# Kernel optimization log

Measured on AMD Instinct MI355X. Metric: run time of the kernel, lower is better.

## Reference

```python
import jax, jax.numpy as jnp
import numpy as np

N = 100000   # nodes
E = 400000   # edges
B = 4000     # graphs
D = 300      # emb_dim
L = 5        # num_layer
MAX_LEN = 50 # max_atom_num (hard-coded in forward)
SELF_LOOP_BOND_TYPE = 4
BN_EPS = 1e-5


def setup_inputs() -> dict:
    key = jax.random.key(0)
    ks = jax.random.split(key, 12)
    x = jax.random.randint(ks[0], (N, 2), 0, 3)            # col0 atom type (<120), col1 chirality (<3)
    edge_index = jax.random.randint(ks[1], (2, E), 0, N)
    edge_attr = jax.random.randint(ks[2], (E, 2), 0, 3)    # col0 bond type (<6), col1 direction (<3)
    batch = jnp.sort(jax.random.randint(ks[3], (N,), 0, B))
    sc = 0.05
    x_emb1 = jax.random.normal(ks[4], (120, D)) * sc
    x_emb2 = jax.random.normal(ks[5], (3, D)) * sc
    e_emb1 = jax.random.normal(ks[6], (L, 6, D)) * sc
    e_emb2 = jax.random.normal(ks[7], (L, 3, D)) * sc
    W1 = jax.random.normal(ks[8], (L, D, 2 * D)) * (1.0 / np.sqrt(D))
    b1 = jnp.zeros((L, 2 * D))
    W2 = jax.random.normal(ks[9], (L, 2 * D, D)) * (1.0 / np.sqrt(2 * D))
    b2 = jnp.zeros((L, D))
    bn_gamma = jnp.ones((L, D))
    bn_beta = jnp.zeros((L, D))
    return dict(x=x, edge_index=edge_index, edge_attr=edge_attr, batch=batch,
                num_graphs=B, x_emb1=x_emb1, x_emb2=x_emb2, e_emb1=e_emb1,
                e_emb2=e_emb2, W1=W1, b1=b1, W2=W2, b2=b2,
                bn_gamma=bn_gamma, bn_beta=bn_beta)


def reference(x, edge_index, edge_attr, batch, num_graphs,
              x_emb1, x_emb2, e_emb1, e_emb2, W1, b1, W2, b2, bn_gamma, bn_beta):
    n = x.shape[0]
    # input node embedding: atom type + chirality
    h = x_emb1[x[:, 0]] + x_emb2[x[:, 1]]  # [N, D]
    # add self loops (bond_type=4, direction=0)
    loop = jnp.arange(n)
    src = jnp.concatenate([edge_index[0], loop])
    dst = jnp.concatenate([edge_index[1], loop])
    ea0 = jnp.concatenate([edge_attr[:, 0], jnp.full((n,), SELF_LOOP_BOND_TYPE, edge_attr.dtype)])
    ea1 = jnp.concatenate([edge_attr[:, 1], jnp.zeros((n,), edge_attr.dtype)])
    num_layers = W1.shape[0]
    for l in range(num_layers):
        ee = e_emb1[l][ea0] + e_emb2[l][ea1]                 # [E+N, D] edge embeddings
        msg = h[src] + ee                                     # gather + message
        agg = jax.ops.segment_sum(msg, dst, num_segments=n)   # scatter-add aggregation
        hid = jax.nn.relu(agg @ W1[l] + b1[l])                # GIN MLP
        h2 = hid @ W2[l] + b2[l]
        mean = h2.mean(axis=0)                                # BatchNorm1d (batch stats, biased var)
        var = jnp.mean((h2 - mean) ** 2, axis=0)
        h2 = (h2 - mean) * jax.lax.rsqrt(var + BN_EPS) * bn_gamma[l] + bn_beta[l]
        # dropout with drop_ratio=0 is identity; relu on all but last layer
        h = h2 if l == num_layers - 1 else jax.nn.relu(h2)
    # global mean pool over graphs
    counts = jax.ops.segment_sum(jnp.ones((n,), h.dtype), batch, num_segments=num_graphs)
    pooled = jax.ops.segment_sum(h, batch, num_segments=num_graphs) / jnp.maximum(counts, 1.0)[:, None]
    # atom_feature_pad: pad per-graph node features to MAX_LEN with mask
    idx = jnp.arange(n)
    is_start = jnp.concatenate([jnp.array([True]), batch[1:] != batch[:-1]])
    start = jax.lax.cummax(jnp.where(is_start, idx, 0))
    pos = idx - start                                          # position within each graph
    valid = pos < MAX_LEN
    posc = jnp.minimum(pos, MAX_LEN - 1)
    d = h.shape[1]
    node_feature = jnp.zeros((num_graphs, MAX_LEN, d), h.dtype).at[batch, posc].add(
        h * valid[:, None].astype(h.dtype))
    mask = jnp.zeros((num_graphs, MAX_LEN), h.dtype).at[batch, posc].add(valid.astype(h.dtype))
    return pooled, node_feature, mask
```

## Files before the change

kernel.cpp:

```cpp
#include <hip/hip_runtime.h>
#include <cstdint>

#define D 300
#define MAXLEN 50
#define K1P 320
#define H1 600
#define H1P 608
#define W1ROWS 640
#define W2ROWS 384

typedef __attribute__((ext_vector_type(8))) short s16x8;
typedef __attribute__((ext_vector_type(4))) short s16x4;
typedef __attribute__((ext_vector_type(4))) float f32x4;
typedef __attribute__((ext_vector_type(2))) float f32x2;
typedef __attribute__((ext_vector_type(4))) int i32x4;

__device__ __forceinline__ unsigned short f2b(float f) {
  uint32_t u = __builtin_bit_cast(uint32_t, f);
  u += 0x7FFFu + ((u >> 16) & 1u);
  return (unsigned short)(u >> 16);
}
__device__ __forceinline__ float b2f(unsigned short s) {
  return __builtin_bit_cast(float, (uint32_t)s << 16);
}
__device__ __forceinline__ void gld_lds16(const void* g, void* l) {
  __builtin_amdgcn_global_load_lds((const __attribute__((address_space(1))) void*)g,
                                   (__attribute__((address_space(3))) void*)l, 16, 0, 0);
}

__global__ void k_cmb(const float* __restrict__ xe1, const float* __restrict__ xe2,
                      unsigned short* __restrict__ cmb, int total ) {
  int i = blockIdx.x * blockDim.x + threadIdx.x;
  if (i >= total) return;
  int c = i / 75, d = (i - c * 75) * 4;
  int a = c / 3, b = c - a * 3;
  s16x4 out;
#pragma unroll
  for (int j = 0; j < 4; ++j) out[j] = (short)f2b(xe1[(size_t)a * D + d + j] + xe2[(size_t)b * D + d + j]);
  *(s16x4*)(cmb + (size_t)c * K1P + d) = out;
}

__global__ void k_cid(const int* __restrict__ x, int* __restrict__ cid, int N) {
  int i = blockIdx.x * blockDim.x + threadIdx.x;
  if (i < N) cid[i] = x[2 * i] * 3 + x[2 * i + 1];
}

__global__ void k_count(const int* __restrict__ key, int* __restrict__ cnt, int n) {
  int i = blockIdx.x * blockDim.x + threadIdx.x;
  if (i < n) atomicAdd(&cnt[key[i]], 1);
}

__global__ void k_scan1(const int* __restrict__ in, int* __restrict__ part, int n) {
  __shared__ int red[256];
  int tid = threadIdx.x;
  int base = blockIdx.x * 1024 + tid * 4;
  i32x4 v = {0, 0, 0, 0};
  if (base + 3 < n) v = *(const i32x4*)(in + base);
  else {
#pragma unroll
    for (int k = 0; k < 4; ++k) v[k] = (base + k < n) ? in[base + k] : 0;
  }
  int s = v[0] + v[1] + v[2] + v[3];
  red[tid] = s;
  __syncthreads();
  for (int off = 1; off < 256; off <<= 1) {
    int t = (tid >= off) ? red[tid - off] : 0;
    __syncthreads();
    red[tid] += t;
    __syncthreads();
  }
  if (tid == 255) part[blockIdx.x] = red[255];
}

__global__ void k_scan2(int* __restrict__ part, int P) {
  __shared__ int sm[1024];
  int tid = threadIdx.x;
  int v = (tid < P) ? part[tid] : 0;
  sm[tid] = v;
  __syncthreads();
  for (int off = 1; off < 1024; off <<= 1) {
    int t = (tid >= off) ? sm[tid - off] : 0;
    __syncthreads();
    sm[tid] += t;
    __syncthreads();
  }
  if (tid < P) part[tid] = sm[tid] - v;
  if (tid == 1023) part[P] = sm[1023];
}

__global__ void k_scan3(const int* __restrict__ in, const int* __restrict__ part,
                        int* __restrict__ out, int n, int P) {
  __shared__ int red[256];
  int tid = threadIdx.x;
  int base = blockIdx.x * 1024 + tid * 4;
  i32x4 v = {0, 0, 0, 0};
  if (base + 3 < n) v = *(const i32x4*)(in + base);
  else {
#pragma unroll
    for (int k = 0; k < 4; ++k) v[k] = (base + k < n) ? in[base + k] : 0;
  }
  int s = v[0] + v[1] + v[2] + v[3];
  red[tid] = s;
  __syncthreads();
  for (int off = 1; off < 256; off <<= 1) {
    int t = (tid >= off) ? red[tid - off] : 0;
    __syncthreads();
    red[tid] += t;
    __syncthreads();
  }
  int pre = red[tid] - s + part[blockIdx.x];
  if (base < n) out[base] = pre;
  if (base + 1 < n) out[base + 1] = pre + v[0];
  if (base + 2 < n) out[base + 2] = pre + v[0] + v[1];
  if (base + 3 < n) out[base + 3] = pre + v[0] + v[1] + v[2];
  if (blockIdx.x == 0 && tid == 0) out[n] = part[P];
}

__global__ void k_fill(const int* __restrict__ src, const int* __restrict__ dst,
                       const int* __restrict__ ea, const int* __restrict__ cid,
                       int* __restrict__ cur, const int* __restrict__ offs,
                       int* __restrict__ ssrc, int* __restrict__ scid,
                       int* __restrict__ cnt18, int E_) {
  int e = blockIdx.x * blockDim.x + threadIdx.x;
  if (e >= E_) return;
  int d = dst[e];
  int s = src[e];
  int p = atomicAdd(&cur[d], 1);
  int pos = offs[d] + p;
  ssrc[pos] = s;
  scid[pos] = cid[s];
  int co = ea[2 * e] * 3 + ea[2 * e + 1];
  atomicAdd(&cnt18[d * 18 + co], 1);
}

__global__ void k_cnt18bf(const int* __restrict__ cnt18, unsigned short* __restrict__ aggbf, int N) {
  int idx = blockIdx.x * blockDim.x + threadIdx.x;
  if (idx >= N * 10) return;
  int i = idx / 10, j = idx - i * 10;
  uint32_t o = 0;
  if (j < 9) {
    int c0 = cnt18[i * 18 + 2 * j] + (2 * j == 12 ? 1 : 0);
    int c1 = cnt18[i * 18 + 2 * j + 1];
    o = (uint32_t)f2b((float)c0) | ((uint32_t)f2b((float)c1) << 16);
  }
  *(uint32_t*)(aggbf + (size_t)i * K1P + D + j * 2) = o;
}

__global__ void k_ecw1(const float* __restrict__ ee1, const float* __restrict__ ee2,
                       const float* __restrict__ W1, unsigned short* __restrict__ W1tA,
                       int L_, int total ) {
  int idx = blockIdx.x * blockDim.x + threadIdx.x;
  if (idx >= total) return;
  int k18 = idx % 18;
  int n = (idx / 18) % H1;
  int l = idx / (18 * H1);
  const float* e1 = ee1 + ((size_t)l * 6 + k18 / 3) * D;
  const float* e2 = ee2 + ((size_t)l * 3 + k18 % 3) * D;
  const float* w = W1 + (size_t)l * D * H1 + n;
  float s = 0.f;
  for (int d = 0; d < D; ++d) s += (e1[d] + e2[d]) * w[(size_t)d * H1];
  W1tA[(size_t)l * W1ROWS * K1P + (size_t)n * K1P + D + k18] = f2b(s);
}

template <int FUSE>
__global__ void k_agg(const unsigned short* __restrict__ hin, const int* __restrict__ ridx,
                      const int* __restrict__ offs, const float* __restrict__ scale,
                      const float* __restrict__ shift, const int* __restrict__ selfcid,
                      unsigned short* __restrict__ aggbf, int N) {
  int w = (int)((blockIdx.x * blockDim.x + threadIdx.x) >> 6);
  if (w >= N) return;
  int lane = threadIdx.x & 63;
  const bool act1 = lane < 11;
  const int e0 = lane * 4;
  const int e1 = (act1 ? (64 + lane) : lane) * 4;
  float sc0[4], sh0[4], sc1[4], sh1[4];
  if (FUSE) {
    f32x4 a = *(const f32x4*)(scale + e0);
    f32x4 b = *(const f32x4*)(shift + e0);
    f32x4 c = *(const f32x4*)(scale + e1);
    f32x4 d = *(const f32x4*)(shift + e1);
#pragma unroll
    for (int j = 0; j < 4; ++j) { sc0[j] = a[j]; sh0[j] = b[j]; sc1[j] = c[j]; sh1[j] = d[j]; }
  } else {
#pragma unroll
    for (int j = 0; j < 4; ++j) { sc0[j] = sc1[j] = sh0[j] = sh1[j] = 0.f; }
  }
  int beg = offs[w], end = offs[w + 1];
  int wrow = FUSE ? w : selfcid[w];
  float s0[4], s1[4];
  {
    const unsigned short* rp = hin + (size_t)wrow * K1P;
    s16x4 v0 = *(const s16x4*)(rp + e0);
    s16x4 v1 = *(const s16x4*)(rp + e1);
#pragma unroll
    for (int j = 0; j < 4; ++j) {
      float a = b2f((unsigned short)v0[j]);
      float b = b2f((unsigned short)v1[j]);
      if (FUSE) { a = fmaxf(a * sc0[j] + sh0[j], 0.f); b = fmaxf(b * sc1[j] + sh1[j], 0.f); }
      s0[j] = a; s1[j] = b;
    }
  }
  int j = beg;
  for (; j + 4 <= end; j += 4) {
    const unsigned short* p0 = hin + (size_t)ridx[j] * K1P;
    const unsigned short* p1 = hin + (size_t)ridx[j + 1] * K1P;
    const unsigned short* p2 = hin + (size_t)ridx[j + 2] * K1P;
    const unsigned short* p3 = hin + (size_t)ridx[j + 3] * K1P;
    s16x4 a0 = *(const s16x4*)(p0 + e0), b0 = *(const s16x4*)(p0 + e1);
    s16x4 a1 = *(const s16x4*)(p1 + e0), b1 = *(const s16x4*)(p1 + e1);
    s16x4 a2 = *(const s16x4*)(p2 + e0), b2 = *(const s16x4*)(p2 + e1);
    s16x4 a3 = *(const s16x4*)(p3 + e0), b3 = *(const s16x4*)(p3 + e1);
#pragma unroll
    for (int k = 0; k < 4; ++k) {
      float x0 = b2f((unsigned short)a0[k]), x1 = b2f((unsigned short)a1[k]);
      float x2 = b2f((unsigned short)a2[k]), x3 = b2f((unsigned short)a3[k]);
      float y0 = b2f((unsigned short)b0[k]), y1 = b2f((unsigned short)b1[k]);
      float y2 = b2f((unsigned short)b2[k]), y3 = b2f((unsigned short)b3[k]);
      if (FUSE) {
        x0 = fmaxf(x0 * sc0[k] + sh0[k], 0.f); x1 = fmaxf(x1 * sc0[k] + sh0[k], 0.f);
        x2 = fmaxf(x2 * sc0[k] + sh0[k], 0.f); x3 = fmaxf(x3 * sc0[k] + sh0[k], 0.f);
        y0 = fmaxf(y0 * sc1[k] + sh1[k], 0.f); y1 = fmaxf(y1 * sc1[k] + sh1[k], 0.f);
        y2 = fmaxf(y2 * sc1[k] + sh1[k], 0.f); y3 = fmaxf(y3 * sc1[k] + sh1[k], 0.f);
      }
      s0[k] += (x0 + x1) + (x2 + x3);
      s1[k] += (y0 + y1) + (y2 + y3);
    }
  }
  for (; j < end; ++j) {
    const unsigned short* rp = hin + (size_t)ridx[j] * K1P;
    s16x4 v0 = *(const s16x4*)(rp + e0);
    s16x4 v1 = *(const s16x4*)(rp + e1);
#pragma unroll
    for (int k = 0; k < 4; ++k) {
      float a = b2f((unsigned short)v0[k]);
      float b = b2f((unsigned short)v1[k]);
      if (FUSE) { a = fmaxf(a * sc0[k] + sh0[k], 0.f); b = fmaxf(b * sc1[k] + sh1[k], 0.f); }
      s0[k] += a;
      s1[k] += b;
    }
  }
  s16x4 o0, o1;
#pragma unroll
  for (int k = 0; k < 4; ++k) { o0[k] = (short)f2b(s0[k]); o1[k] = (short)f2b(s1[k]); }
  *(s16x4*)(aggbf + (size_t)w * K1P + e0) = o0;
  if (act1) *(s16x4*)(aggbf + (size_t)w * K1P + e1) = o1;
}

__global__ void k_wconv(const float* __restrict__ W, unsigned short* __restrict__ Wt,
                        int K, int Nout, int Kp, int total) {
  int idx = blockIdx.x * blockDim.x + threadIdx.x;
  if (idx >= total) return;
  int n = idx / Kp, k = idx - n * Kp;
  float v = (k < K && n < Nout) ? W[(size_t)k * Nout + n] : 0.f;
  Wt[idx] = f2b(v);
}

template <int K, int EPI>
__global__ __launch_bounds__(256, 3) void k_gemm(
    const unsigned short* __restrict__ A, const unsigned short* __restrict__ Bt,
    const float* __restrict__ bias, unsigned short* __restrict__ Cb,
    float* __restrict__ sums, int M, int Nout, int ldc, int CT) {
  constexpr int T = K / 32;
  __shared__ __align__(16) unsigned short smem[24576];

  int nwg = gridDim.x;
  int q = nwg >> 3, r8 = nwg & 7;
  int xcd = blockIdx.x & 7, oidx = blockIdx.x >> 3;
  int wid = (xcd < r8 ? xcd * (q + 1) : r8 * (q + 1) + (xcd - r8) * q) + oidx;
  int ct = wid % CT, rt = wid / CT;
  const int rowBase = rt * 128, colBase = ct * 128;

  const int tid = threadIdx.x, lane = tid & 63, wave = tid >> 6;
  const int wm = wave >> 1, wn = wave & 1;
  const int l15 = lane & 15, lg = lane >> 4;

  unsigned short* Asm = smem;
  unsigned short* Bsm = smem + 12288;

  auto stage = [&](int s, int t) {
#pragma unroll
    for (int i = 0; i < 2; ++i) {
      int u = tid + i * 256;
      int rr = u >> 2;
      int cdat = (u & 3) ^ ((rr >> 1) & 3);
      int gr = rowBase + rr; if (gr >= M) gr = M - 1;
      gld_lds16(A + (size_t)gr * K + t * 32 + cdat * 8, Asm + s * 4096 + u * 8);
      gld_lds16(Bt + (size_t)(colBase + rr) * K + t * 32 + cdat * 8, Bsm + s * 4096 + u * 8);
    }
  };

  f32x4 acc[4][4] = {};
  stage(0, 0);
  stage(1, 1);
#pragma unroll
  for (int t = 0; t < T; ++t) {
    if (t + 1 < T) asm volatile("s_waitcnt vmcnt(4)" ::: "memory");
    else           asm volatile("s_waitcnt vmcnt(0)" ::: "memory");
    __builtin_amdgcn_s_barrier();
    __builtin_amdgcn_sched_barrier(0);
    const unsigned short* bA = Asm + (t % 3) * 4096;
    const unsigned short* bB = Bsm + (t % 3) * 4096;
    s16x8 af[4], bf[4];
#pragma unroll
    for (int i = 0; i < 4; ++i) {
      int ra = wm * 64 + i * 16 + l15;
      int rb = wn * 64 + i * 16 + l15;
      af[i] = *(const s16x8*)(bA + ((size_t)ra * 4 + (lg ^ ((ra >> 1) & 3))) * 8);
      bf[i] = *(const s16x8*)(bB + ((size_t)rb * 4 + (lg ^ ((rb >> 1) & 3))) * 8);
    }
    if (t + 2 < T) stage((t + 2) % 3, t + 2);
#pragma unroll
    for (int mi = 0; mi < 4; ++mi)
#pragma unroll
      for (int ni = 0; ni < 4; ++ni)
        acc[mi][ni] = __builtin_amdgcn_mfma_f32_16x16x32_bf16(af[mi], bf[ni], acc[mi][ni], 0, 0, 0);
  }

  float bnS[4] = {0.f, 0.f, 0.f, 0.f}, bnQ[4] = {0.f, 0.f, 0.f, 0.f};
#pragma unroll
  for (int ni = 0; ni < 4; ++ni) {
    int col = colBase + wn * 64 + ni * 16 + l15;
    if (col >= (EPI ? ldc : Nout)) continue;
    bool inN = col < Nout;
    float bv = inN ? bias[col] : 0.f;
#pragma unroll
    for (int mi = 0; mi < 4; ++mi) {
      int row0 = rowBase + wm * 64 + mi * 16 + lg * 4;
#pragma unroll
      for (int rr = 0; rr < 4; ++rr) {
        int row = row0 + rr;
        if (row < M) {
          float v = inN ? acc[mi][ni][rr] + bv : 0.f;
          if (EPI) v = fmaxf(v, 0.f);
          else { bnS[ni] += v; bnQ[ni] += v * v; }
          Cb[(size_t)row * ldc + col] = f2b(v);
        }
      }
    }
  }
  if (!EPI) {
#pragma unroll
    for (int ni = 0; ni < 4; ++ni) {
      float cs = bnS[ni], cq = bnQ[ni];
      cs += __shfl_xor(cs, 16); cq += __shfl_xor(cq, 16);
      cs += __shfl_xor(cs, 32); cq += __shfl_xor(cq, 32);
      int col = colBase + wn * 64 + ni * 16 + l15;
      if (lg == 0 && col < Nout) {
        atomicAdd(&sums[col], cs);
        atomicAdd(&sums[D + col], cq);
      }
    }
  }
}

__global__ void k_bnfinal(const float* __restrict__ sums, const float* __restrict__ sumsq,
                          const float* __restrict__ gamma, const float* __restrict__ beta,
                          float* __restrict__ scale, float* __restrict__ shift, int N) {
  int c = threadIdx.x;
  if (c >= D) return;
  float inv = 1.f / (float)N;
  float mean = sums[c] * inv;
  float var = sumsq[c] * inv - mean * mean;
  if (var < 0.f) var = 0.f;
  float sc = gamma[c] * rsqrtf(var + 1e-5f);
  scale[c] = sc;
  shift[c] = beta[c] - mean * sc;
}

__global__ void k_pool(const unsigned short* __restrict__ hb, const float* __restrict__ scale,
                       const float* __restrict__ shift, const int* __restrict__ gs,
                       const int* __restrict__ gc, float* __restrict__ pooled, int total ) {
  int gid = blockIdx.x * blockDim.x + threadIdx.x;
  if (gid >= total) return;
  int g = gid / 75, c4 = (gid - g * 75) * 4;
  int start = gs[g], cnt = gc[g];
  f32x4 s = {0.f, 0.f, 0.f, 0.f};
  for (int i = 0; i < cnt; ++i) {
    s16x4 in = *(const s16x4*)(hb + (size_t)(start + i) * K1P + c4);
#pragma unroll
    for (int j = 0; j < 4; ++j) s[j] += b2f((unsigned short)in[j]);
  }
  f32x4 sc = *(const f32x4*)(scale + c4);
  f32x4 sh = *(const f32x4*)(shift + c4);
  float dv = (cnt > 0) ? (float)cnt : 1.f;
  f32x4 out;
#pragma unroll
  for (int j = 0; j < 4; ++j) out[j] = (s[j] * sc[j] + sh[j] * (float)cnt) / dv;
  *(f32x4*)(pooled + (size_t)g * D + c4) = out;
}

__global__ void k_nf(const unsigned short* __restrict__ hb, const float* __restrict__ scale,
                     const float* __restrict__ shift, const int* __restrict__ gs,
                     const int* __restrict__ gc, float* __restrict__ nf, float* __restrict__ mask) {
  int g = blockIdx.x;
  int start = gs[g], cnt = gc[g];
  int lim = cnt < MAXLEN ? cnt : MAXLEN;
  for (int idx = threadIdx.x; idx < MAXLEN * 75; idx += 256) {
    int p = idx / 75;
    int c4 = (idx - p * 75) * 4;
    f32x4 v = {0.f, 0.f, 0.f, 0.f};
    if (p < lim) {
      s16x4 in = *(const s16x4*)(hb + (size_t)(start + p) * K1P + c4);
      f32x4 sc = *(const f32x4*)(scale + c4);
      f32x4 sh = *(const f32x4*)(shift + c4);
#pragma unroll
      for (int j = 0; j < 4; ++j) v[j] = b2f((unsigned short)in[j]) * sc[j] + sh[j];
    }
    *(f32x4*)(nf + (size_t)g * (MAXLEN * D) + p * D + c4) = v;
  }
  if (threadIdx.x < MAXLEN) mask[(size_t)g * MAXLEN + threadIdx.x] = (threadIdx.x < lim) ? 1.f : 0.f;
}

extern "C" void kernel_launch(void* const* d_in, const int* in_sizes, int n_in,
                              void* d_out, int out_size, void* d_ws, size_t ws_size,
                              hipStream_t stream) {
  const int* x      = (const int*)d_in[0];
  const int* ei     = (const int*)d_in[1];
  const int* ea     = (const int*)d_in[2];
  const int* batch  = (const int*)d_in[3];
  const float* xe1  = (const float*)d_in[5];
  const float* xe2  = (const float*)d_in[6];
  const float* ee1  = (const float*)d_in[7];
  const float* ee2  = (const float*)d_in[8];
  const float* W1   = (const float*)d_in[9];
  const float* b1   = (const float*)d_in[10];
  const float* W2   = (const float*)d_in[11];
  const float* b2   = (const float*)d_in[12];
  const float* gamma = (const float*)d_in[13];
  const float* beta  = (const float*)d_in[14];

  const int N = in_sizes[0] / 2;
  const int E = in_sizes[1] / 2;
  const int L = in_sizes[9] / (D * 2 * D);
  const int B = out_size / (D + MAXLEN * D + MAXLEN);

  char* ws = (char*)d_ws;
  size_t off = 0;
  auto alloc = [&](size_t bytes) -> void* {
    void* p = ws + off;
    off += (bytes + 255) & ~(size_t)255;
    return p;
  };
  unsigned short* aggbf = (unsigned short*)alloc((size_t)N * K1P * 2);
  unsigned short* hb    = (unsigned short*)alloc((size_t)N * K1P * 2);
  unsigned short* hid   = (unsigned short*)alloc((size_t)N * H1P * 2);
  unsigned short* cmb   = (unsigned short*)alloc((size_t)360 * K1P * 2);
  unsigned short* W1tA = (unsigned short*)alloc((size_t)L * W1ROWS * K1P * 2);
  unsigned short* W2tA = (unsigned short*)alloc((size_t)L * W2ROWS * H1P * 2);
  int* cnt    = (int*)alloc((size_t)N * 4);
  int* cur    = (int*)alloc((size_t)N * 4);
  int* offs   = (int*)alloc((size_t)(N + 1) * 4);
  int* cid    = (int*)alloc((size_t)N * 4);
  int* cnt18  = (int*)alloc((size_t)N * 18 * 4);
  int* ssrc   = (int*)alloc((size_t)E * 4);
  int* scid   = (int*)alloc((size_t)E * 4);
  int* gc     = (int*)alloc((size_t)B * 4);
  int* gs     = (int*)alloc((size_t)(B + 1) * 4);
  int* part   = (int*)alloc(1024 * 4);
  float* sumsA = (float*)alloc((size_t)L * 2 * D * 4);
  float* scale = (float*)alloc(2 * D * 4);

  hipMemsetAsync(cnt, 0, (size_t)N * 4, stream);
  hipMemsetAsync(cur, 0, (size_t)N * 4, stream);
  hipMemsetAsync(gc, 0, (size_t)B * 4, stream);
  hipMemsetAsync(cnt18, 0, (size_t)N * 18 * 4, stream);
  hipMemsetAsync(sumsA, 0, (size_t)L * 2 * D * 4, stream);

  k_cmb<<<(360 * 75 + 255) / 256, 256, 0, stream>>>(xe1, xe2, cmb, 360 * 75);
  k_cid<<<(N + 255) / 256, 256, 0, stream>>>(x, cid, N);
  k_count<<<(E + 255) / 256, 256, 0, stream>>>(ei + E, cnt, E);
  {
    int P = (N + 1023) / 1024;
    k_scan1<<<P, 256, 0, stream>>>(cnt, part, N);
    k_scan2<<<1, 1024, 0, stream>>>(part, P);
    k_scan3<<<P, 256, 0, stream>>>(cnt, part, offs, N, P);
  }
  k_fill<<<(E + 255) / 256, 256, 0, stream>>>(ei, ei + E, ea, cid, cur, offs, ssrc, scid, cnt18, E);
  k_cnt18bf<<<(N * 10 + 255) / 256, 256, 0, stream>>>(cnt18, aggbf, N);
  k_count<<<(N + 255) / 256, 256, 0, stream>>>(batch, gc, N);
  {
    int P = (B + 1023) / 1024;
    k_scan1<<<P, 256, 0, stream>>>(gc, part, B);
    k_scan2<<<1, 1024, 0, stream>>>(part, P);
    k_scan3<<<P, 256, 0, stream>>>(gc, part, gs, B, P);
  }
  for (int l = 0; l < L; ++l) {
    k_wconv<<<(W1ROWS * K1P + 255) / 256, 256, 0, stream>>>(
        W1 + (size_t)l * D * H1, W1tA + (size_t)l * W1ROWS * K1P, D, H1, K1P, W1ROWS * K1P);
    k_wconv<<<(W2ROWS * H1P + 255) / 256, 256, 0, stream>>>(
        W2 + (size_t)l * H1 * D, W2tA + (size_t)l * W2ROWS * H1P, H1, D, H1P, W2ROWS * H1P);
  }
  k_ecw1<<<(L * H1 * 18 + 255) / 256, 256, 0, stream>>>(ee1, ee2, W1, W1tA, L, L * H1 * 18);

  const int RT = (N + 127) / 128;
  for (int l = 0; l < L; ++l) {
    float* sums = sumsA + (size_t)l * 2 * D;
    if (l == 0)
      k_agg<0><<<(N + 3) / 4, 256, 0, stream>>>(cmb, scid, offs, nullptr, nullptr, cid, aggbf, N);
    else
      k_agg<1><<<(N + 3) / 4, 256, 0, stream>>>(hb, ssrc, offs, scale, scale + D, nullptr, aggbf, N);
    k_gemm<K1P, 1><<<5 * RT, 256, 0, stream>>>(
        aggbf, W1tA + (size_t)l * W1ROWS * K1P, b1 + (size_t)l * H1, hid, nullptr, N, H1, H1P, 5);
    k_gemm<H1P, 0><<<3 * RT, 256, 0, stream>>>(
        hid, W2tA + (size_t)l * W2ROWS * H1P, b2 + (size_t)l * D, hb, sums, N, D, K1P, 3);
    k_bnfinal<<<1, 320, 0, stream>>>(sums, sums + D, gamma + (size_t)l * D, beta + (size_t)l * D,
                                     scale, scale + D, N);
  }

  float* out = (float*)d_out;
  float* out_pooled = out;
  float* out_nf = out + (size_t)B * D;
  float* out_mask = out + (size_t)B * D + (size_t)B * MAXLEN * D;
  k_pool<<<(B * 75 + 255) / 256, 256, 0, stream>>>(hb, scale, scale + D, gs, gc, out_pooled, B * 75);
  k_nf<<<B, 256, 0, stream>>>(hb, scale, scale + D, gs, gc, out_nf, out_mask);
}
```

Baseline: 1.676 ms.

## Load GEMM A operand directly from global into registers, bypassing LDS

The A tile in the MFMA GEMM was staged through LDS with global-to-LDS copies. It is now loaded per lane straight from global memory into registers, double-buffered two k-steps ahead, while B keeps the triple-buffered LDS path. This halves LDS traffic and footprint, which may allow more resident blocks. In exchange, A rows are re-fetched by both wn waves, global reads become less coalesced (16 bytes per lane per row), and the vmcnt wait accounting changes.

```diff
diff --git a/kernel.cpp b/kernel.cpp
--- a/kernel.cpp
+++ b/kernel.cpp
@@ -261,7 +261,7 @@
     const float* __restrict__ bias, unsigned short* __restrict__ Cb,
     float* __restrict__ sums, int M, int Nout, int ldc, int CT) {
   constexpr int T = K / 32;
-  __shared__ __align__(16) unsigned short smem[24576];
+  __shared__ __align__(16) unsigned short Bsm[3 * 4096];
 
   int nwg = gridDim.x;
   int q = nwg >> 3, r8 = nwg & 7;
@@ -274,46 +274,56 @@
   const int wm = wave >> 1, wn = wave & 1;
   const int l15 = lane & 15, lg = lane >> 4;
 
-  unsigned short* Asm = smem;
-  unsigned short* Bsm = smem + 12288;
-
-  auto stage = [&](int s, int t) {
+  const unsigned short* Arow[4];
+#pragma unroll
+  for (int mi = 0; mi < 4; ++mi) {
+    int r = rowBase + wm * 64 + mi * 16 + l15;
+    if (r >= M) r = M - 1;
+    Arow[mi] = A + (size_t)r * K + lg * 8;
+  }
+
+  auto stageB = [&](int s, int t) {
 #pragma unroll
     for (int i = 0; i < 2; ++i) {
       int u = tid + i * 256;
       int rr = u >> 2;
       int cdat = (u & 3) ^ ((rr >> 1) & 3);
-      int gr = rowBase + rr; if (gr >= M) gr = M - 1;
-      gld_lds16(A + (size_t)gr * K + t * 32 + cdat * 8, Asm + s * 4096 + u * 8);
       gld_lds16(Bt + (size_t)(colBase + rr) * K + t * 32 + cdat * 8, Bsm + s * 4096 + u * 8);
     }
   };
 
+  s16x8 aset[2][4];
+#pragma unroll
+  for (int mi = 0; mi < 4; ++mi) aset[0][mi] = *(const s16x8*)(Arow[mi]);
+  stageB(0, 0);
+#pragma unroll
+  for (int mi = 0; mi < 4; ++mi) aset[1][mi] = *(const s16x8*)(Arow[mi] + 32);
+  stageB(1, 1);
+
   f32x4 acc[4][4] = {};
-  stage(0, 0);
-  stage(1, 1);
 #pragma unroll
   for (int t = 0; t < T; ++t) {
-    if (t + 1 < T) asm volatile("s_waitcnt vmcnt(4)" ::: "memory");
+    if (t + 1 < T) asm volatile("s_waitcnt vmcnt(6)" ::: "memory");
     else           asm volatile("s_waitcnt vmcnt(0)" ::: "memory");
     __builtin_amdgcn_s_barrier();
     __builtin_amdgcn_sched_barrier(0);
-    const unsigned short* bA = Asm + (t % 3) * 4096;
     const unsigned short* bB = Bsm + (t % 3) * 4096;
-    s16x8 af[4], bf[4];
+    s16x8 bf[4];
 #pragma unroll
     for (int i = 0; i < 4; ++i) {
-      int ra = wm * 64 + i * 16 + l15;
       int rb = wn * 64 + i * 16 + l15;
-      af[i] = *(const s16x8*)(bA + ((size_t)ra * 4 + (lg ^ ((ra >> 1) & 3))) * 8);
       bf[i] = *(const s16x8*)(bB + ((size_t)rb * 4 + (lg ^ ((rb >> 1) & 3))) * 8);
     }
-    if (t + 2 < T) stage((t + 2) % 3, t + 2);
 #pragma unroll
     for (int mi = 0; mi < 4; ++mi)
 #pragma unroll
       for (int ni = 0; ni < 4; ++ni)
-        acc[mi][ni] = __builtin_amdgcn_mfma_f32_16x16x32_bf16(af[mi], bf[ni], acc[mi][ni], 0, 0, 0);
+        acc[mi][ni] = __builtin_amdgcn_mfma_f32_16x16x32_bf16(aset[t & 1][mi], bf[ni], acc[mi][ni], 0, 0, 0);
+    if (t + 2 < T) {
+#pragma unroll
+      for (int mi = 0; mi < 4; ++mi) aset[t & 1][mi] = *(const s16x8*)(Arow[mi] + (t + 2) * 32);
+      stageB((t + 2) % 3, t + 2);
+    }
   }
 
   float bnS[4] = {0.f, 0.f, 0.f, 0.f}, bnQ[4] = {0.f, 0.f, 0.f, 0.f};
```

Measured after the change: 1.922 ms. +14.7%, slower.
